# Kernel optimization log

Measured on AMD Instinct MI355X. Metric: run time of the kernel, lower is better.

The kernel has to match this reference:

```python
import jax, jax.numpy as jnp
import numpy as np

B, T, C, H = 4096, 64, 128, 64  # batch, seq (== blok_olcusu), embed (yerlesdirme_olcusu), head size


def setup_inputs() -> dict:
    key = jax.random.key(0)
    kx, kq, kk, kv = jax.random.split(key, 4)
    x = jax.random.normal(kx, (B, T, C), dtype=jnp.float32)
    # Linear(C, H, bias=False); stored as [in, out] so projection is x @ W
    Wq = jax.random.normal(kq, (C, H), dtype=jnp.float32) * (C ** -0.5)
    Wk = jax.random.normal(kk, (C, H), dtype=jnp.float32) * (C ** -0.5)
    Wv = jax.random.normal(kv, (C, H), dtype=jnp.float32) * (C ** -0.5)
    return {"x": x, "Wq": Wq, "Wk": Wk, "Wv": Wv}


def reference(x, Wq, Wk, Wv):
    _, t, c = x.shape
    q = jnp.einsum("btc,ch->bth", x, Wq)
    k = jnp.einsum("btc,ch->bth", x, Wk)
    v = jnp.einsum("btc,ch->bth", x, Wv)
    # NOTE: source scales by C**-0.5 where C is the EMBEDDING dim, not head size
    scores = jnp.einsum("bth,bsh->bts", q, k) * (c ** -0.5)  # [B, T, T]
    causal = jnp.tril(jnp.ones((t, t), dtype=bool))
    scores = jnp.where(causal, scores, -jnp.inf)
    attn = jax.nn.softmax(scores, axis=-1)
    # dropout is identity in eval mode
    out = jnp.einsum("bts,bsh->bth", attn, v)  # [B, T, H]
    return out
```

## Files before the change

### kernel.cpp

```cpp
#include <hip/hip_runtime.h>
#include <stdint.h>

#define NB 4096
#define TT 64
#define CC 128
#define HH 64
#define BPB 4

typedef __bf16 bf16x8 __attribute__((ext_vector_type(8)));
typedef float f32x4 __attribute__((ext_vector_type(4)));
typedef unsigned short us4 __attribute__((ext_vector_type(4)));

__device__ __forceinline__ unsigned short f2bf(float f) {
  union { float f; uint32_t u; } a; a.f = f;
  uint32_t u = a.u;
  u += 0x7fffu + ((u >> 16) & 1u);
  return (unsigned short)(u >> 16);
}

__device__ __forceinline__ unsigned short bfbits(float f) {
  union { __bf16 b; unsigned short u; } c; c.b = (__bf16)f; return c.u;
}

__global__ void swizzle_w_kernel(const float* __restrict__ Wq,
                                 const float* __restrict__ Wk,
                                 const float* __restrict__ Wv,
                                 unsigned short* __restrict__ wz) {
  int i = blockIdx.x * 256 + threadIdx.x;
  if (i >= 3 * 16 * 64) return;
  int mat  = i >> 10;
  int rem  = i & 1023;
  int frag = rem >> 6;
  int lane = rem & 63;
  int nt = frag >> 2, ks = frag & 3;
  int quad = lane >> 4, l15 = lane & 15;
  int h  = nt * 16 + l15;
  int c0 = ks * 32 + quad * 8;
  const float* W = (mat == 0) ? Wq : (mat == 1) ? Wk : Wv;
  unsigned short* o = wz + (size_t)i * 8;
  #pragma unroll
  for (int j = 0; j < 8; ++j) o[j] = f2bf(W[(c0 + j) * HH + h]);
}

#define MFMA16(A, B, C) __builtin_amdgcn_mfma_f32_16x16x32_bf16((A), (B), (C), 0, 0, 0)

__global__ __launch_bounds__(256, 2)
void attn_kernel(const float* __restrict__ x,
                 const unsigned short* __restrict__ wz,
                 float* __restrict__ out) {
  __shared__ unsigned short xs [64 * 128];
  __shared__ unsigned short qs [64 * 64];
  __shared__ unsigned short ks_[64 * 64];
  __shared__ unsigned short vts[64 * 64];

  const int tid  = threadIdx.x;
  const int wave = tid >> 6;
  const int lane = tid & 63;
  const int quad = lane >> 4;
  const int l15  = lane & 15;
  const int l7   = l15 & 7;
  const int mbase = wave * 16;
  const float scale = 0.08838834764831845f;

  const unsigned short* wb = wz + (size_t)lane * 8;
#define WLOAD(P, K) (*(const bf16x8*)(wb + ((size_t)((wave * 3 + (P)) * 4 + (K)) << 9)))
  bf16x8 w00 = WLOAD(0, 0), w01 = WLOAD(0, 1), w02 = WLOAD(0, 2), w03 = WLOAD(0, 3);
  bf16x8 w10 = WLOAD(1, 0), w11 = WLOAD(1, 1), w12 = WLOAD(1, 2), w13 = WLOAD(1, 3);
  bf16x8 w20 = WLOAD(2, 0), w21 = WLOAD(2, 1), w22 = WLOAD(2, 2), w23 = WLOAD(2, 3);
#undef WLOAD

  const int b0 = blockIdx.x * BPB;

  for (int bi = 0; bi < BPB; ++bi) {
    const int b = b0 + bi;
    if (bi > 0) __syncthreads();

    #pragma unroll
    for (int k = 0; k < 4; ++k) {
      const int i = tid + 256 * k;
      const int row = i >> 4, c = i & 15;
      const float* src = x + ((size_t)b * TT + row) * CC + c * 8;
      const f32x4 lo = *(const f32x4*)src;
      const f32x4 hi = *(const f32x4*)(src + 4);
      bf16x8 v;
      #pragma unroll
      for (int j = 0; j < 4; ++j) { v[j] = (__bf16)lo[j]; v[j + 4] = (__bf16)hi[j]; }
      *(bf16x8*)&xs[row * 128 + ((c ^ (row & 7)) << 3)] = v;
    }
    __syncthreads();

    #pragma unroll
    for (int mt = 0; mt < 4; ++mt) {
#define XLOAD(K) (*(const bf16x8*)&xs[(mt * 16 + l15) * 128 + (((((K) << 2) + quad) ^ l7) << 3)])
      const bf16x8 xf0 = XLOAD(0), xf1 = XLOAD(1), xf2 = XLOAD(2), xf3 = XLOAD(3);
#undef XLOAD
#define PROJ(P) do {                                                         \
      f32x4 acc_ = {0.f, 0.f, 0.f, 0.f};                                     \
      acc_ = MFMA16(xf0, w##P##0, acc_);                                     \
      acc_ = MFMA16(xf1, w##P##1, acc_);                                     \
      acc_ = MFMA16(xf2, w##P##2, acc_);                                     \
      acc_ = MFMA16(xf3, w##P##3, acc_);                                     \
      const int pi_ = wave * 3 + (P);                                        \
      const int mat_ = pi_ >> 2, nt_ = pi_ & 3;                              \
      if (mat_ == 2) {                                                       \
            \
        const int h_  = (nt_ << 4) + l15;                                    \
        const int t0_ = (mt << 4) + (quad << 2);                             \
        us4 pk_;                                                             \
        pk_[0] = bfbits(acc_[0]); pk_[1] = bfbits(acc_[1]);                  \
        pk_[2] = bfbits(acc_[2]); pk_[3] = bfbits(acc_[3]);                  \
        *(us4*)&vts[(h_ << 6) + (((t0_ >> 3) ^ (h_ & 7)) << 3) + (t0_ & 7)] = pk_; \
      } else {                                                               \
        unsigned short* dst_ = (mat_ == 0) ? qs : ks_;                       \
        const int col_ = (nt_ << 4) + l15;                                   \
        const int ch_ = col_ >> 3, cj_ = col_ & 7;                           \
        _Pragma("unroll")                                                    \
        for (int r_ = 0; r_ < 4; ++r_) {                                     \
          const int row_ = (mt << 4) + (quad << 2) + r_;                     \
          dst_[(row_ << 6) + ((ch_ ^ (row_ & 7)) << 3) + cj_] = bfbits(acc_[r_]); \
        }                                                                    \
      }                                                                      \
    } while (0)
      PROJ(0); PROJ(1); PROJ(2);
#undef PROJ
    }
    __syncthreads();

    const bf16x8 aq0 = *(const bf16x8*)&qs[((mbase + l15) << 6) + ((quad ^ l7) << 3)];
    const bf16x8 aq1 = *(const bf16x8*)&qs[((mbase + l15) << 6) + (((4 + quad) ^ l7) << 3)];
    f32x4 sc0 = {0.f, 0.f, 0.f, 0.f}, sc1 = sc0, sc2 = sc0, sc3 = sc0;
#define QK(NT, SC) do {                                                                          \
      const bf16x8 bk0_ = *(const bf16x8*)&ks_[((((NT) << 4) + l15) << 6) + ((quad ^ l7) << 3)]; \
      const bf16x8 bk1_ = *(const bf16x8*)&ks_[((((NT) << 4) + l15) << 6) + (((4 + quad) ^ l7) << 3)]; \
      SC = MFMA16(aq0, bk0_, SC);                                                                \
      SC = MFMA16(aq1, bk1_, SC);                                                                \
    } while (0)
    QK(0, sc0); QK(1, sc1); QK(2, sc2); QK(3, sc3);
#undef QK
    #pragma unroll
    for (int r = 0; r < 4; ++r) {
      const int row = mbase + (quad << 2) + r;
      float v0 = (l15      <= row) ? sc0[r] * scale : -__builtin_inff();
      float v1 = (l15 + 16 <= row) ? sc1[r] * scale : -__builtin_inff();
      float v2 = (l15 + 32 <= row) ? sc2[r] * scale : -__builtin_inff();
      float v3 = (l15 + 48 <= row) ? sc3[r] * scale : -__builtin_inff();
      float m = fmaxf(fmaxf(v0, v1), fmaxf(v2, v3));
      #pragma unroll
      for (int d = 1; d < 16; d <<= 1) m = fmaxf(m, __shfl_xor(m, d, 64));
      v0 = __expf(v0 - m); v1 = __expf(v1 - m); v2 = __expf(v2 - m); v3 = __expf(v3 - m);
      float s = (v0 + v1) + (v2 + v3);
      #pragma unroll
      for (int d = 1; d < 16; d <<= 1) s += __shfl_xor(s, d, 64);
      const float inv = 1.f / s;
      const int rs = row & 7;
      qs[(row << 6) + (((l15 >> 3)     ^ rs) << 3) + (l15 & 7)] = bfbits(v0 * inv);
      qs[(row << 6) + ((((l15 >> 3) + 2) ^ rs) << 3) + (l15 & 7)] = bfbits(v1 * inv);
      qs[(row << 6) + ((((l15 >> 3) + 4) ^ rs) << 3) + (l15 & 7)] = bfbits(v2 * inv);
      qs[(row << 6) + ((((l15 >> 3) + 6) ^ rs) << 3) + (l15 & 7)] = bfbits(v3 * inv);
    }

    const bf16x8 ap0 = *(const bf16x8*)&qs[((mbase + l15) << 6) + ((quad ^ l7) << 3)];
    const bf16x8 ap1 = *(const bf16x8*)&qs[((mbase + l15) << 6) + (((4 + quad) ^ l7) << 3)];
    float* ob = out + (size_t)b * TT * HH;
#define PV(NT) do {                                                                              \
      const bf16x8 bv0_ = *(const bf16x8*)&vts[((((NT) << 4) + l15) << 6) + ((quad ^ l7) << 3)]; \
      const bf16x8 bv1_ = *(const bf16x8*)&vts[((((NT) << 4) + l15) << 6) + (((4 + quad) ^ l7) << 3)]; \
      f32x4 acc_ = {0.f, 0.f, 0.f, 0.f};                                                         \
      acc_ = MFMA16(ap0, bv0_, acc_);                                                            \
      acc_ = MFMA16(ap1, bv1_, acc_);                                                            \
      _Pragma("unroll")                                                                          \
      for (int r_ = 0; r_ < 4; ++r_)                                                             \
        ob[(mbase + (quad << 2) + r_) * HH + ((NT) << 4) + l15] = acc_[r_];                      \
    } while (0)
    PV(0); PV(1); PV(2); PV(3);
#undef PV
  }
}

extern "C" void kernel_launch(void* const* d_in, const int* in_sizes, int n_in,
                              void* d_out, int out_size, void* d_ws, size_t ws_size,
                              hipStream_t stream) {
  const float* x  = (const float*)d_in[0];
  const float* Wq = (const float*)d_in[1];
  const float* Wk = (const float*)d_in[2];
  const float* Wv = (const float*)d_in[3];
  unsigned short* wz = (unsigned short*)d_ws;
  float* outp = (float*)d_out;

  swizzle_w_kernel<<<(3 * 16 * 64 + 255) / 256, 256, 0, stream>>>(Wq, Wk, Wv, wz);
  attn_kernel<<<NB / BPB, 256, 0, stream>>>(x, wz, outp);
}
```

Before: 223.3 us.

## Double-buffer QKV projection and load x directly into MFMA registers

The x tile is no longer staged through shared memory. Each wave loads fp32 x rows straight from global memory into registers and converts them to bf16 MFMA fragments. Q/K/V shared buffers are double-buffered, so the projection for the next batch element is issued before the attention of the current one, leaving one barrier per iteration instead of three. This costs more shared memory (3x2x8KB) and register pressure, and x is read with less coalesced per-lane strided accesses.

```diff
diff --git a/kernel.cpp b/kernel.cpp
--- a/kernel.cpp
+++ b/kernel.cpp
@@ -20,6 +20,13 @@
 
 __device__ __forceinline__ unsigned short bfbits(float f) {
   union { __bf16 b; unsigned short u; } c; c.b = (__bf16)f; return c.u;
+}
+
+__device__ __forceinline__ bf16x8 cv8(f32x4 lo, f32x4 hi) {
+  bf16x8 v;
+  #pragma unroll
+  for (int j = 0; j < 4; ++j) { v[j] = (__bf16)lo[j]; v[j + 4] = (__bf16)hi[j]; }
+  return v;
 }
 
 __global__ void swizzle_w_kernel(const float* __restrict__ Wq,
@@ -48,10 +55,9 @@
 void attn_kernel(const float* __restrict__ x,
                  const unsigned short* __restrict__ wz,
                  float* __restrict__ out) {
-  __shared__ unsigned short xs [64 * 128];
-  __shared__ unsigned short qs [64 * 64];
-  __shared__ unsigned short ks_[64 * 64];
-  __shared__ unsigned short vts[64 * 64];
+  __shared__ unsigned short qbuf[2][64 * 64];
+  __shared__ unsigned short kbuf[2][64 * 64];
+  __shared__ unsigned short vbuf[2][64 * 64];
 
   const int tid  = threadIdx.x;
   const int wave = tid >> 6;
@@ -69,111 +75,113 @@
   bf16x8 w20 = WLOAD(2, 0), w21 = WLOAD(2, 1), w22 = WLOAD(2, 2), w23 = WLOAD(2, 3);
 #undef WLOAD
 
+#define PROJ1(P, MT, QSB, KSB, VTB) do {                                     \
+    f32x4 acc_ = {0.f, 0.f, 0.f, 0.f};                                       \
+    acc_ = MFMA16(xf0_, w##P##0, acc_);                                      \
+    acc_ = MFMA16(xf1_, w##P##1, acc_);                                      \
+    acc_ = MFMA16(xf2_, w##P##2, acc_);                                      \
+    acc_ = MFMA16(xf3_, w##P##3, acc_);                                      \
+    const int pi_ = wave * 3 + (P);                                          \
+    const int mat_ = pi_ >> 2, nt_ = pi_ & 3;                                \
+    if (mat_ == 2) {                                                         \
+                   \
+      const int h_  = (nt_ << 4) + l15;                                      \
+      const int t0_ = ((MT) << 4) + (quad << 2);                             \
+      us4 pk_;                                                               \
+      pk_[0] = bfbits(acc_[0]); pk_[1] = bfbits(acc_[1]);                    \
+      pk_[2] = bfbits(acc_[2]); pk_[3] = bfbits(acc_[3]);                    \
+      *(us4*)&(VTB)[(h_ << 6) + (((t0_ >> 3) ^ (h_ & 7)) << 3) + (t0_ & 7)] = pk_; \
+    } else {                                                                 \
+      unsigned short* dst_ = (mat_ == 0) ? (QSB) : (KSB);                    \
+      const int col_ = (nt_ << 4) + l15;                                     \
+      const int ch_ = col_ >> 3, cj_ = col_ & 7;                             \
+      _Pragma("unroll")                                                      \
+      for (int r_ = 0; r_ < 4; ++r_) {                                       \
+        const int row_ = ((MT) << 4) + (quad << 2) + r_;                     \
+        (dst_)[(row_ << 6) + ((ch_ ^ (row_ & 7)) << 3) + cj_] = bfbits(acc_[r_]); \
+      }                                                                      \
+    }                                                                        \
+  } while (0)
+
+#define DO_PROJ(BB, QSB, KSB, VTB) do {                                      \
+    _Pragma("unroll")                                                        \
+    for (int mt_ = 0; mt_ < 4; ++mt_) {                                      \
+      const float* xr_ = x + ((size_t)(BB) * TT + mt_ * 16 + l15) * CC + quad * 8; \
+      const f32x4 a0_ = *(const f32x4*)(xr_);       const f32x4 b0_ = *(const f32x4*)(xr_ + 4);  \
+      const f32x4 a1_ = *(const f32x4*)(xr_ + 32);  const f32x4 b1_ = *(const f32x4*)(xr_ + 36); \
+      const f32x4 a2_ = *(const f32x4*)(xr_ + 64);  const f32x4 b2_ = *(const f32x4*)(xr_ + 68); \
+      const f32x4 a3_ = *(const f32x4*)(xr_ + 96);  const f32x4 b3_ = *(const f32x4*)(xr_ + 100);\
+      const bf16x8 xf0_ = cv8(a0_, b0_), xf1_ = cv8(a1_, b1_);               \
+      const bf16x8 xf2_ = cv8(a2_, b2_), xf3_ = cv8(a3_, b3_);               \
+      PROJ1(0, mt_, QSB, KSB, VTB);                                          \
+      PROJ1(1, mt_, QSB, KSB, VTB);                                          \
+      PROJ1(2, mt_, QSB, KSB, VTB);                                          \
+    }                                                                        \
+  } while (0)
+
+#define QK1(NT, SC, KSB) do {                                                \
+    const bf16x8 bk0_ = *(const bf16x8*)&(KSB)[((((NT) << 4) + l15) << 6) + ((quad ^ l7) << 3)]; \
+    const bf16x8 bk1_ = *(const bf16x8*)&(KSB)[((((NT) << 4) + l15) << 6) + (((4 + quad) ^ l7) << 3)]; \
+    SC = MFMA16(aq0_, bk0_, SC);                                             \
+    SC = MFMA16(aq1_, bk1_, SC);                                             \
+  } while (0)
+
+#define PV1(NT, QSB, VTB) do {                                               \
+    const bf16x8 bv0_ = *(const bf16x8*)&(VTB)[((((NT) << 4) + l15) << 6) + ((quad ^ l7) << 3)]; \
+    const bf16x8 bv1_ = *(const bf16x8*)&(VTB)[((((NT) << 4) + l15) << 6) + (((4 + quad) ^ l7) << 3)]; \
+    f32x4 acc_ = {0.f, 0.f, 0.f, 0.f};                                       \
+    acc_ = MFMA16(ap0_, bv0_, acc_);                                         \
+    acc_ = MFMA16(ap1_, bv1_, acc_);                                         \
+    _Pragma("unroll")                                                        \
+    for (int r_ = 0; r_ < 4; ++r_)                                           \
+      ob_[(mbase + (quad << 2) + r_) * HH + ((NT) << 4) + l15] = acc_[r_];   \
+  } while (0)
+
+#define DO_ATTN(BB, QSB, KSB, VTB) do {                                      \
+    const bf16x8 aq0_ = *(const bf16x8*)&(QSB)[((mbase + l15) << 6) + ((quad ^ l7) << 3)]; \
+    const bf16x8 aq1_ = *(const bf16x8*)&(QSB)[((mbase + l15) << 6) + (((4 + quad) ^ l7) << 3)]; \
+    f32x4 sc0_ = {0.f, 0.f, 0.f, 0.f}, sc1_ = sc0_, sc2_ = sc0_, sc3_ = sc0_; \
+    QK1(0, sc0_, KSB); QK1(1, sc1_, KSB); QK1(2, sc2_, KSB); QK1(3, sc3_, KSB); \
+    _Pragma("unroll")                                                        \
+    for (int r_ = 0; r_ < 4; ++r_) {                                         \
+      const int row_ = mbase + (quad << 2) + r_;                             \
+      float v0_ = (l15      <= row_) ? sc0_[r_] * scale : -__builtin_inff(); \
+      float v1_ = (l15 + 16 <= row_) ? sc1_[r_] * scale : -__builtin_inff(); \
+      float v2_ = (l15 + 32 <= row_) ? sc2_[r_] * scale : -__builtin_inff(); \
+      float v3_ = (l15 + 48 <= row_) ? sc3_[r_] * scale : -__builtin_inff(); \
+      float m_ = fmaxf(fmaxf(v0_, v1_), fmaxf(v2_, v3_));                    \
+      _Pragma("unroll")                                                      \
+      for (int d_ = 1; d_ < 16; d_ <<= 1) m_ = fmaxf(m_, __shfl_xor(m_, d_, 64)); \
+      v0_ = __expf(v0_ - m_); v1_ = __expf(v1_ - m_);                        \
+      v2_ = __expf(v2_ - m_); v3_ = __expf(v3_ - m_);                        \
+      float s_ = (v0_ + v1_) + (v2_ + v3_);                                  \
+      _Pragma("unroll")                                                      \
+      for (int d_ = 1; d_ < 16; d_ <<= 1) s_ += __shfl_xor(s_, d_, 64);      \
+      const float inv_ = 1.f / s_;                                           \
+      const int rs_ = row_ & 7;                                              \
+       \
+      (QSB)[(row_ << 6) + ((( (l15 >> 3)    ) ^ rs_) << 3) + (l15 & 7)] = bfbits(v0_ * inv_); \
+      (QSB)[(row_ << 6) + ((((l15 >> 3) + 2) ^ rs_) << 3) + (l15 & 7)] = bfbits(v1_ * inv_); \
+      (QSB)[(row_ << 6) + ((((l15 >> 3) + 4) ^ rs_) << 3) + (l15 & 7)] = bfbits(v2_ * inv_); \
+      (QSB)[(row_ << 6) + ((((l15 >> 3) + 6) ^ rs_) << 3) + (l15 & 7)] = bfbits(v3_ * inv_); \
+    }                                                                        \
+    const bf16x8 ap0_ = *(const bf16x8*)&(QSB)[((mbase + l15) << 6) + ((quad ^ l7) << 3)]; \
+    const bf16x8 ap1_ = *(const bf16x8*)&(QSB)[((mbase + l15) << 6) + (((4 + quad) ^ l7) << 3)]; \
+    float* ob_ = out + (size_t)(BB) * TT * HH;                               \
+    PV1(0, QSB, VTB); PV1(1, QSB, VTB); PV1(2, QSB, VTB); PV1(3, QSB, VTB);  \
+  } while (0)
+
   const int b0 = blockIdx.x * BPB;
 
+  DO_PROJ(b0, qbuf[0], kbuf[0], vbuf[0]);
+  __syncthreads();
+
+  #pragma unroll
   for (int bi = 0; bi < BPB; ++bi) {
-    const int b = b0 + bi;
-    if (bi > 0) __syncthreads();
-
-    #pragma unroll
-    for (int k = 0; k < 4; ++k) {
-      const int i = tid + 256 * k;
-      const int row = i >> 4, c = i & 15;
-      const float* src = x + ((size_t)b * TT + row) * CC + c * 8;
-      const f32x4 lo = *(const f32x4*)src;
-      const f32x4 hi = *(const f32x4*)(src + 4);
-      bf16x8 v;
-      #pragma unroll
-      for (int j = 0; j < 4; ++j) { v[j] = (__bf16)lo[j]; v[j + 4] = (__bf16)hi[j]; }
-      *(bf16x8*)&xs[row * 128 + ((c ^ (row & 7)) << 3)] = v;
-    }
+    const int cu_ = bi & 1;
+    if (bi < BPB - 1) DO_PROJ(b0 + bi + 1, qbuf[cu_ ^ 1], kbuf[cu_ ^ 1], vbuf[cu_ ^ 1]);
+    DO_ATTN(b0 + bi, qbuf[cu_], kbuf[cu_], vbuf[cu_]);
     __syncthreads();
-
-    #pragma unroll
-    for (int mt = 0; mt < 4; ++mt) {
-#define XLOAD(K) (*(const bf16x8*)&xs[(mt * 16 + l15) * 128 + (((((K) << 2) + quad) ^ l7) << 3)])
-      const bf16x8 xf0 = XLOAD(0), xf1 = XLOAD(1), xf2 = XLOAD(2), xf3 = XLOAD(3);
-#undef XLOAD
-#define PROJ(P) do {                                                         \
-      f32x4 acc_ = {0.f, 0.f, 0.f, 0.f};                                     \
-      acc_ = MFMA16(xf0, w##P##0, acc_);                                     \
-      acc_ = MFMA16(xf1, w##P##1, acc_);                                     \
-      acc_ = MFMA16(xf2, w##P##2, acc_);                                     \
-      acc_ = MFMA16(xf3, w##P##3, acc_);                                     \
-      const int pi_ = wave * 3 + (P);                                        \
-      const int mat_ = pi_ >> 2, nt_ = pi_ & 3;                              \
-      if (mat_ == 2) {                                                       \
-            \
-        const int h_  = (nt_ << 4) + l15;                                    \
-        const int t0_ = (mt << 4) + (quad << 2);                             \
-        us4 pk_;                                                             \
-        pk_[0] = bfbits(acc_[0]); pk_[1] = bfbits(acc_[1]);                  \
-        pk_[2] = bfbits(acc_[2]); pk_[3] = bfbits(acc_[3]);                  \
-        *(us4*)&vts[(h_ << 6) + (((t0_ >> 3) ^ (h_ & 7)) << 3) + (t0_ & 7)] = pk_; \
-      } else {                                                               \
-        unsigned short* dst_ = (mat_ == 0) ? qs : ks_;                       \
-        const int col_ = (nt_ << 4) + l15;                                   \
-        const int ch_ = col_ >> 3, cj_ = col_ & 7;                           \
-        _Pragma("unroll")                                                    \
-        for (int r_ = 0; r_ < 4; ++r_) {                                     \
-          const int row_ = (mt << 4) + (quad << 2) + r_;                     \
-          dst_[(row_ << 6) + ((ch_ ^ (row_ & 7)) << 3) + cj_] = bfbits(acc_[r_]); \
-        }                                                                    \
-      }                                                                      \
-    } while (0)
-      PROJ(0); PROJ(1); PROJ(2);
-#undef PROJ
-    }
-    __syncthreads();
-
-    const bf16x8 aq0 = *(const bf16x8*)&qs[((mbase + l15) << 6) + ((quad ^ l7) << 3)];
-    const bf16x8 aq1 = *(const bf16x8*)&qs[((mbase + l15) << 6) + (((4 + quad) ^ l7) << 3)];
-    f32x4 sc0 = {0.f, 0.f, 0.f, 0.f}, sc1 = sc0, sc2 = sc0, sc3 = sc0;
-#define QK(NT, SC) do {                                                                          \
-      const bf16x8 bk0_ = *(const bf16x8*)&ks_[((((NT) << 4) + l15) << 6) + ((quad ^ l7) << 3)]; \
-      const bf16x8 bk1_ = *(const bf16x8*)&ks_[((((NT) << 4) + l15) << 6) + (((4 + quad) ^ l7) << 3)]; \
-      SC = MFMA16(aq0, bk0_, SC);                                                                \
-      SC = MFMA16(aq1, bk1_, SC);                                                                \
-    } while (0)
-    QK(0, sc0); QK(1, sc1); QK(2, sc2); QK(3, sc3);
-#undef QK
-    #pragma unroll
-    for (int r = 0; r < 4; ++r) {
-      const int row = mbase + (quad << 2) + r;
-      float v0 = (l15      <= row) ? sc0[r] * scale : -__builtin_inff();
-      float v1 = (l15 + 16 <= row) ? sc1[r] * scale : -__builtin_inff();
-      float v2 = (l15 + 32 <= row) ? sc2[r] * scale : -__builtin_inff();
-      float v3 = (l15 + 48 <= row) ? sc3[r] * scale : -__builtin_inff();
-      float m = fmaxf(fmaxf(v0, v1), fmaxf(v2, v3));
-      #pragma unroll
-      for (int d = 1; d < 16; d <<= 1) m = fmaxf(m, __shfl_xor(m, d, 64));
-      v0 = __expf(v0 - m); v1 = __expf(v1 - m); v2 = __expf(v2 - m); v3 = __expf(v3 - m);
-      float s = (v0 + v1) + (v2 + v3);
-      #pragma unroll
-      for (int d = 1; d < 16; d <<= 1) s += __shfl_xor(s, d, 64);
-      const float inv = 1.f / s;
-      const int rs = row & 7;
-      qs[(row << 6) + (((l15 >> 3)     ^ rs) << 3) + (l15 & 7)] = bfbits(v0 * inv);
-      qs[(row << 6) + ((((l15 >> 3) + 2) ^ rs) << 3) + (l15 & 7)] = bfbits(v1 * inv);
-      qs[(row << 6) + ((((l15 >> 3) + 4) ^ rs) << 3) + (l15 & 7)] = bfbits(v2 * inv);
-      qs[(row << 6) + ((((l15 >> 3) + 6) ^ rs) << 3) + (l15 & 7)] = bfbits(v3 * inv);
-    }
-
-    const bf16x8 ap0 = *(const bf16x8*)&qs[((mbase + l15) << 6) + ((quad ^ l7) << 3)];
-    const bf16x8 ap1 = *(const bf16x8*)&qs[((mbase + l15) << 6) + (((4 + quad) ^ l7) << 3)];
-    float* ob = out + (size_t)b * TT * HH;
-#define PV(NT) do {                                                                              \
-      const bf16x8 bv0_ = *(const bf16x8*)&vts[((((NT) << 4) + l15) << 6) + ((quad ^ l7) << 3)]; \
-      const bf16x8 bv1_ = *(const bf16x8*)&vts[((((NT) << 4) + l15) << 6) + (((4 + quad) ^ l7) << 3)]; \
-      f32x4 acc_ = {0.f, 0.f, 0.f, 0.f};                                                         \
-      acc_ = MFMA16(ap0, bv0_, acc_);                                                            \
-      acc_ = MFMA16(ap1, bv1_, acc_);                                                            \
-      _Pragma("unroll")                                                                          \
-      for (int r_ = 0; r_ < 4; ++r_)                                                             \
-        ob[(mbase + (quad << 2) + r_) * HH + ((NT) << 4) + l15] = acc_[r_];                      \
-    } while (0)
-    PV(0); PV(1); PV(2); PV(3);
-#undef PV
   }
 }
 
```

New measurement: 251.5 us. +12.6%, slower.
